# Kernel optimization log

Hardware: AMD Instinct MI355X
Metric: run time of the kernel (lower is better)

Reference implementation:

```python
import jax, jax.numpy as jnp
import numpy as np

SEQ, BATCH, HID, NLAYERS = 2048, 16, 1024, 2


def setup_inputs() -> dict:
    key = jax.random.key(0)
    ks = jax.random.split(key, 3)
    scale = 1.0 / np.sqrt(HID)
    x = jax.random.normal(ks[0], (SEQ, BATCH, HID), dtype=jnp.float32)
    W0 = jax.random.normal(ks[1], (HID, 3 * HID), dtype=jnp.float32) * scale
    b0 = jnp.zeros((2 * HID,), dtype=jnp.float32)
    W1 = jax.random.normal(ks[2], (HID, 3 * HID), dtype=jnp.float32) * scale
    b1 = jnp.zeros((2 * HID,), dtype=jnp.float32)
    return {"x": x, "W0": W0, "b0": b0, "W1": W1, "b1": b1}


def _sru_layer(x, W, b):
    # x: [L, B, H]; W: [H, 3H]; b: [2H]
    L, B, H = x.shape
    U = jnp.einsum('lbd,dk->lbk', x, W)  # [L, B, 3H]
    x_tilde = U[..., :H]
    bf, br = b[:H], b[H:]
    f = jax.nn.sigmoid(U[..., H:2 * H] + bf)  # forget gate [L,B,H]
    r = jax.nn.sigmoid(U[..., 2 * H:] + br)   # reset gate  [L,B,H]

    def step(c_prev, inp):
        xt_t, f_t = inp
        c_t = f_t * c_prev + (1.0 - f_t) * xt_t
        return c_t, c_t

    c0 = jnp.zeros((B, H), dtype=x.dtype)
    _, cs = jax.lax.scan(step, c0, (x_tilde, f))  # cs: [L, B, H]
    h = r * cs + (1.0 - r) * x  # highway connection
    return h


def reference(x, W0, b0, W1, b1):
    h = _sru_layer(x, W0, b0)
    h = _sru_layer(h, W1, b1)
    return h[-1:]  # [1, B, H], matching `out[-1:]`
```

## Files before the change

### kernel.cpp

```cpp
#include <hip/hip_runtime.h>

#define SEQ    2048
#define BATCH  16
#define HID    1024
#define M_TOT  (SEQ*BATCH)
#define NCH    (BATCH*HID)
#define NCHUNK 32
#define TCHUNK (SEQ/NCHUNK)

typedef __attribute__((ext_vector_type(8))) short          short8;
typedef __attribute__((ext_vector_type(8))) unsigned short ushort8_t;
typedef __attribute__((ext_vector_type(4))) float          floatx4;

__device__ __forceinline__ unsigned short f32_to_bf16(float f) {
  unsigned int u = __float_as_uint(f);
  u += 0x7FFFu + ((u >> 16) & 1u);
  return (unsigned short)(u >> 16);
}
__device__ __forceinline__ float bf16_to_f32(unsigned short h) {
  return __uint_as_float(((unsigned int)h) << 16);
}
__device__ __forceinline__ float sigmoidf_(float x) {
  return 1.f / (1.f + __expf(-x));
}


__device__ __forceinline__ void cast_swizzle_body(const float* __restrict__ src,
    unsigned short* __restrict__ dst, int mt, int kt, int t) {
  __shared__ unsigned short tile[4096];
  const int r = t >> 1, kh = (t & 1) * 16;
  const float* sp = src + (size_t)(mt * 128 + r) * 1024 + kt * 32 + kh;
  float4 v0 = *(const float4*)(sp + 0);
  float4 v1 = *(const float4*)(sp + 4);
  float4 v2 = *(const float4*)(sp + 8);
  float4 v3 = *(const float4*)(sp + 12);
  ushort8_t u0, u1;
  u0[0]=f32_to_bf16(v0.x); u0[1]=f32_to_bf16(v0.y); u0[2]=f32_to_bf16(v0.z); u0[3]=f32_to_bf16(v0.w);
  u0[4]=f32_to_bf16(v1.x); u0[5]=f32_to_bf16(v1.y); u0[6]=f32_to_bf16(v1.z); u0[7]=f32_to_bf16(v1.w);
  u1[0]=f32_to_bf16(v2.x); u1[1]=f32_to_bf16(v2.y); u1[2]=f32_to_bf16(v2.z); u1[3]=f32_to_bf16(v2.w);
  u1[4]=f32_to_bf16(v3.x); u1[5]=f32_to_bf16(v3.y); u1[6]=f32_to_bf16(v3.z); u1[7]=f32_to_bf16(v3.w);
  const int c = r >> 4, lr = r & 15, q0 = kh >> 3;
  const int unit0 = c * 64 + (q0 << 4) + lr;
  *(ushort8_t*)&tile[unit0 * 8]        = u0;
  *(ushort8_t*)&tile[(unit0 + 16) * 8] = u1;
  __syncthreads();
  const size_t base = ((size_t)mt * 32 + kt) * 4096;
  *(ushort8_t*)&dst[base + t * 16]     = *(const ushort8_t*)&tile[t * 16];
  *(ushort8_t*)&dst[base + t * 16 + 8] = *(const ushort8_t*)&tile[t * 16 + 8];
}

__device__ __forceinline__ void w_prep_body(const float* __restrict__ W,
    unsigned short* __restrict__ Wsw, int nt, int kt, int t) {
  __shared__ unsigned short tile[4096];
  const int kk = t >> 3, n0 = (t & 7) * 16;
  const float* sp = W + (size_t)(kt * 32 + kk) * 3072 + nt * 128 + n0;
  float v[16];
#pragma unroll
  for (int i = 0; i < 16; i += 4) {
    float4 f = *(const float4*)(sp + i);
    v[i] = f.x; v[i+1] = f.y; v[i+2] = f.z; v[i+3] = f.w;
  }
  const int cbase = (n0 >> 4) * 64 + ((kk >> 3) << 4);
#pragma unroll
  for (int j = 0; j < 16; j++)
    tile[(cbase + j) * 8 + (kk & 7)] = f32_to_bf16(v[j]);
  __syncthreads();
  const size_t base = ((size_t)nt * 32 + kt) * 4096;
  *(ushort8_t*)&Wsw[base + t * 16]     = *(const ushort8_t*)&tile[t * 16];
  *(ushort8_t*)&Wsw[base + t * 16 + 8] = *(const ushort8_t*)&tile[t * 16 + 8];
}

__global__ __launch_bounds__(256) void prep_all(const float* __restrict__ x,
    const float* __restrict__ W0, const float* __restrict__ W1,
    unsigned short* __restrict__ xsw, unsigned short* __restrict__ W0sw,
    unsigned short* __restrict__ W1sw) {
  const int id = blockIdx.x, t = threadIdx.x;
  if (id < 8192)        cast_swizzle_body(x, xsw, id >> 5, id & 31, t);
  else if (id < 8960)   w_prep_body(W0, W0sw, (id - 8192) >> 5, (id - 8192) & 31, t);
  else                  w_prep_body(W1, W1sw, (id - 8960) >> 5, (id - 8960) & 31, t);
}

__global__ __launch_bounds__(256, 2) void gemm_direct(
    const unsigned short* __restrict__ A, const unsigned short* __restrict__ B,
    unsigned short* __restrict__ Xt, unsigned short* __restrict__ Fo, unsigned short* __restrict__ Ro,
    const float* __restrict__ bias, int NBN2)
{
  const int tid = threadIdx.x;
  const int wave = tid >> 6, lane = tid & 63;
  const int wm = wave & 1, wn = wave >> 1;
  const int id = blockIdx.x;
  const int xcd = id & 7, slot = id >> 3;
  const int NB8 = NBN2 << 3;
  const int g = slot / NB8, rem = slot - g * NB8;
  const int bn = rem >> 3;
  const int bm = xcd * 32 + g * 8 + (rem & 7);

  const unsigned short* gA = A + (size_t)bm * 32 * 4096 + wm * 2048 + lane * 8;
  const unsigned short* gB = B + ((size_t)(bn * 2 + wn)) * 32 * 4096 + lane * 8;

  floatx4 acc[4][8];
#pragma unroll
  for (int i = 0; i < 4; i++)
#pragma unroll
    for (int j = 0; j < 8; j++)
#pragma unroll
      for (int r = 0; r < 4; r++) acc[i][j][r] = 0.f;

  short8 a0[4], b0[8], a1[4], b1[8];
  auto loadA = [&](short8* d, const unsigned short* p) {
#pragma unroll
    for (int i = 0; i < 4; i++) d[i] = *(const short8*)(p + i * 512);
  };
  auto loadB = [&](short8* d, const unsigned short* p) {
#pragma unroll
    for (int j = 0; j < 8; j++) d[j] = *(const short8*)(p + j * 512);
  };
  auto domfma = [&](short8* a, short8* b) {
#pragma unroll
    for (int i = 0; i < 4; i++)
#pragma unroll
      for (int j = 0; j < 8; j++)
        acc[i][j] = __builtin_amdgcn_mfma_f32_16x16x32_bf16(a[i], b[j], acc[i][j], 0, 0, 0);
  };

  loadA(a0, gA); loadB(b0, gB);
#pragma unroll 1
  for (int kt = 0; kt < 32; kt += 2) {
    loadA(a1, gA + 4096); loadB(b1, gB + 4096);
    domfma(a0, b0);
    gA += 8192; gB += 8192;
    if (kt + 2 < 32) { loadA(a0, gA); loadB(b0, gB); }
    domfma(a1, b1);
  }

  const int region = bn >> 2;
  const int lc = (bn & 3) * 256 + wn * 128 + (lane & 15);
  const int row0 = bm * 128 + wm * 64 + ((lane >> 4) << 2);
  if (region == 0) {
#pragma unroll
    for (int i = 0; i < 4; i++)
#pragma unroll
      for (int j = 0; j < 8; j++)
#pragma unroll
        for (int rg = 0; rg < 4; rg++)
          Xt[(size_t)(row0 + i * 16 + rg) * 1024 + lc + j * 16] = f32_to_bf16(acc[i][j][rg]);
  } else {
    unsigned short* O = (region == 1) ? Fo : Ro;
    const float* bp = bias + (region - 1) * 1024;
#pragma unroll
    for (int j = 0; j < 8; j++) {
      float bb = bp[lc + j * 16];
#pragma unroll
      for (int i = 0; i < 4; i++)
#pragma unroll
        for (int rg = 0; rg < 4; rg++) {
          float s = sigmoidf_(acc[i][j][rg] + bb);
          O[(size_t)(row0 + i * 16 + rg) * 1024 + lc + j * 16] = f32_to_bf16(s);
        }
    }
  }
}

__global__ __launch_bounds__(256) void scan_pass1(
    const unsigned short* __restrict__ Xt, const unsigned short* __restrict__ F,
    float* __restrict__ P, float* __restrict__ S) {
  const int ch = (blockIdx.x * 256 + threadIdx.x) * 8;
  const int chunk = blockIdx.y;
  size_t idx = (size_t)chunk * TCHUNK * NCH + ch;
  float p[8], s[8];
#pragma unroll
  for (int j = 0; j < 8; j++) { p[j] = 1.f; s[j] = 0.f; }
  for (int t = 0; t < TCHUNK; ++t) {
    ushort8_t fv = *(const ushort8_t*)&F[idx];
    ushort8_t xv = *(const ushort8_t*)&Xt[idx];
#pragma unroll
    for (int j = 0; j < 8; j++) {
      float f  = bf16_to_f32(fv[j]);
      float xt = bf16_to_f32(xv[j]);
      s[j] = f * s[j] + (1.f - f) * xt;
      p[j] *= f;
    }
    idx += NCH;
  }
  float4* P4 = (float4*)&P[(size_t)chunk * NCH + ch];
  float4* S4 = (float4*)&S[(size_t)chunk * NCH + ch];
  P4[0] = make_float4(p[0], p[1], p[2], p[3]);
  P4[1] = make_float4(p[4], p[5], p[6], p[7]);
  S4[0] = make_float4(s[0], s[1], s[2], s[3]);
  S4[1] = make_float4(s[4], s[5], s[6], s[7]);
}

__global__ __launch_bounds__(256) void combine_c0(
    const float* __restrict__ P, const float* __restrict__ S, float* __restrict__ C0) {
  const int ch = (blockIdx.x * 256 + threadIdx.x) * 8;
  float c[8];
#pragma unroll
  for (int j = 0; j < 8; j++) c[j] = 0.f;
  for (int k = 0; k < NCHUNK; ++k) {
    float4* O4 = (float4*)&C0[(size_t)k * NCH + ch];
    O4[0] = make_float4(c[0], c[1], c[2], c[3]);
    O4[1] = make_float4(c[4], c[5], c[6], c[7]);
    const float4* P4 = (const float4*)&P[(size_t)k * NCH + ch];
    const float4* S4 = (const float4*)&S[(size_t)k * NCH + ch];
    float4 p0 = P4[0], p1 = P4[1], s0 = S4[0], s1 = S4[1];
    c[0] = p0.x*c[0]+s0.x; c[1] = p0.y*c[1]+s0.y; c[2] = p0.z*c[2]+s0.z; c[3] = p0.w*c[3]+s0.w;
    c[4] = p1.x*c[4]+s1.x; c[5] = p1.y*c[5]+s1.y; c[6] = p1.z*c[6]+s1.z; c[7] = p1.w*c[7]+s1.w;
  }
}

#define TPAD 4112
__global__ __launch_bounds__(256) void scan1_pass2_fused(
    const unsigned short* __restrict__ Xt, const unsigned short* __restrict__ F,
    const unsigned short* __restrict__ R, unsigned short* __restrict__ xsw,
    const float* __restrict__ C0, unsigned short* __restrict__ h1last)
{
  __shared__ unsigned short st[4 * TPAD];
  const int hb = blockIdx.x;
  const int chunk = blockIdx.y;
  const int tid = threadIdx.x;
  const int b = tid >> 4, hg = tid & 15;
  const int h0 = hb * 128 + hg * 8;
  const int ch = b * 1024 + h0;
  const int tl   = hg >> 2;
  const int usub = (hg & 3) * 16 + b;

  float c[8];
  {
    const float4* C4 = (const float4*)&C0[(size_t)chunk * NCH + ch];
    float4 a = C4[0], d = C4[1];
    c[0]=a.x; c[1]=a.y; c[2]=a.z; c[3]=a.w; c[4]=d.x; c[5]=d.y; c[6]=d.z; c[7]=d.w;
  }

  size_t idx = (size_t)chunk * TCHUNK * NCH + ch;
  for (int t8 = 0; t8 < 8; ++t8) {
#pragma unroll
    for (int ts = 0; ts < 8; ++ts) {
      const int t = chunk * TCHUNK + t8 * 8 + ts;
      ushort8_t fv = *(const ushort8_t*)&F[idx];
      ushort8_t xv = *(const ushort8_t*)&Xt[idx];
      ushort8_t rv = *(const ushort8_t*)&R[idx];
      const size_t soff = ((size_t)(t >> 3) * 32 + (h0 >> 5)) * 4096
                        + (size_t)(((t & 7) * 64 + usub) * 8);
      ushort8_t xo = *(const ushort8_t*)&xsw[soff];
      ushort8_t hv;
#pragma unroll
      for (int j = 0; j < 8; ++j) {
        float f  = bf16_to_f32(fv[j]);
        float xt = bf16_to_f32(xv[j]);
        c[j] = f * c[j] + (1.f - f) * xt;
        float r  = bf16_to_f32(rv[j]);
        float xval = bf16_to_f32(xo[j]);
        hv[j] = f32_to_bf16(r * c[j] + (1.f - r) * xval);
      }
      *(ushort8_t*)&st[tl * TPAD + (ts * 64 + usub) * 8] = hv;
      if (t == SEQ - 1) *(ushort8_t*)&h1last[ch] = hv;
      idx += NCH;
    }
    __syncthreads();
    const size_t gbase = (((size_t)chunk * 8 + t8) * 32 + hb * 4) * 4096;
#pragma unroll
    for (int tl2 = 0; tl2 < 4; ++tl2) {
      size_t gdst = gbase + (size_t)tl2 * 4096 + tid * 16;
      *(ushort8_t*)&xsw[gdst]     = *(const ushort8_t*)&st[tl2 * TPAD + tid * 16];
      *(ushort8_t*)&xsw[gdst + 8] = *(const ushort8_t*)&st[tl2 * TPAD + tid * 16 + 8];
    }
    __syncthreads();
  }
}

__global__ __launch_bounds__(256) void r2_kernel(
    const unsigned short* __restrict__ h1last, const float* __restrict__ W1,
    const float* __restrict__ b1, float* __restrict__ r2) {
  __shared__ float xrow[1024];
  const int b = blockIdx.x, nq = blockIdx.y, tid = threadIdx.x;
  for (int i = tid; i < 1024; i += 256)
    xrow[i] = bf16_to_f32(h1last[b * 1024 + i]);
  __syncthreads();
  const int n = nq * 256 + tid;
  float acc = b1[1024 + n];
  for (int d = 0; d < 1024; ++d)
    acc += xrow[d] * W1[(size_t)d * 3072 + 2048 + n];
  r2[b * 1024 + n] = sigmoidf_(acc);
}

__global__ __launch_bounds__(256) void combine_final(
    const float* __restrict__ P, const float* __restrict__ S,
    const float* __restrict__ r2, const unsigned short* __restrict__ h1last,
    float* __restrict__ out) {
  const int ch = (blockIdx.x * 256 + threadIdx.x) * 8;
  float c[8];
#pragma unroll
  for (int j = 0; j < 8; j++) c[j] = 0.f;
  for (int k = 0; k < NCHUNK; ++k) {
    const float4* P4 = (const float4*)&P[(size_t)k * NCH + ch];
    const float4* S4 = (const float4*)&S[(size_t)k * NCH + ch];
    float4 p0 = P4[0], p1 = P4[1], s0 = S4[0], s1 = S4[1];
    c[0] = p0.x*c[0]+s0.x; c[1] = p0.y*c[1]+s0.y; c[2] = p0.z*c[2]+s0.z; c[3] = p0.w*c[3]+s0.w;
    c[4] = p1.x*c[4]+s1.x; c[5] = p1.y*c[5]+s1.y; c[6] = p1.z*c[6]+s1.z; c[7] = p1.w*c[7]+s1.w;
  }
  const float4* R4 = (const float4*)&r2[ch];
  float4 r0 = R4[0], r1 = R4[1];
  ushort8_t hx = *(const ushort8_t*)&h1last[ch];
  float o[8];
  float rr[8] = {r0.x, r0.y, r0.z, r0.w, r1.x, r1.y, r1.z, r1.w};
#pragma unroll
  for (int j = 0; j < 8; j++)
    o[j] = rr[j] * c[j] + (1.f - rr[j]) * bf16_to_f32(hx[j]);
  float4* O4 = (float4*)&out[ch];
  O4[0] = make_float4(o[0], o[1], o[2], o[3]);
  O4[1] = make_float4(o[4], o[5], o[6], o[7]);
}

extern "C" void kernel_launch(void* const* d_in, const int* in_sizes, int n_in,
                              void* d_out, int out_size, void* d_ws, size_t ws_size,
                              hipStream_t stream) {
  const float* x  = (const float*)d_in[0];
  const float* W0 = (const float*)d_in[1];
  const float* b0 = (const float*)d_in[2];
  const float* W1 = (const float*)d_in[3];
  const float* b1 = (const float*)d_in[4];
  float* out = (float*)d_out;

  char* ws = (char*)d_ws;
  auto alloc = [&](size_t bytes) {
    char* p = ws; ws += (bytes + 255) & ~(size_t)255; return p;
  };
  const size_t NE = (size_t)M_TOT * HID;
  unsigned short* xsw   = (unsigned short*)alloc(NE * 2);
  unsigned short* W0sw  = (unsigned short*)alloc((size_t)3072 * 1024 * 2);
  unsigned short* W1sw  = (unsigned short*)alloc((size_t)3072 * 1024 * 2);
  unsigned short* Xt    = (unsigned short*)alloc(NE * 2);
  unsigned short* F     = (unsigned short*)alloc(NE * 2);
  unsigned short* R     = (unsigned short*)alloc(NE * 2);
  unsigned short* h1last= (unsigned short*)alloc((size_t)NCH * 2);
  float* P   = (float*)alloc((size_t)NCHUNK * NCH * 4);
  float* S   = (float*)alloc((size_t)NCHUNK * NCH * 4);
  float* C0  = (float*)alloc((size_t)NCHUNK * NCH * 4);
  float* r2  = (float*)alloc((size_t)NCH * 4);

  dim3 blk256(256);
  prep_all<<<dim3(9728), blk256, 0, stream>>>(x, W0, W1, xsw, W0sw, W1sw);
  gemm_direct<<<dim3(256 * 12), blk256, 0, stream>>>(xsw, W0sw, Xt, F, R, b0, 12);
  scan_pass1<<<dim3(8, NCHUNK), blk256, 0, stream>>>(Xt, F, P, S);
  combine_c0<<<dim3(8), blk256, 0, stream>>>(P, S, C0);
  scan1_pass2_fused<<<dim3(8, NCHUNK), blk256, 0, stream>>>(Xt, F, R, xsw, C0, h1last);
  gemm_direct<<<dim3(256 * 8), blk256, 0, stream>>>(xsw, W1sw, Xt, F, R, b1, 8);
  r2_kernel<<<dim3(16, 4), blk256, 0, stream>>>(h1last, W1, b1, r2);
  scan_pass1<<<dim3(8, NCHUNK), blk256, 0, stream>>>(Xt, F, P, S);
  combine_final<<<dim3(8), blk256, 0, stream>>>(P, S, r2, h1last, out);
}
```

Baseline: 833.9 us.

## Fuse layer-2 GEMM with segment scan to skip storing gate tensors

Replaces the second-layer GEMM plus scan_pass1 with a kernel that computes only the x_tilde and forget-gate columns, applies the sigmoid and reduces each 32-row tile to a per-segment (product, scan) pair in registers and shared memory. This avoids writing and rereading the full Xt and F tensors. The final kernel then combines 256 segments instead of 32 chunks. The change also raises the occupancy hint on gemm_direct from 2 to 3, which may pressure registers.

```diff
diff --git a/kernel.cpp b/kernel.cpp
--- a/kernel.cpp
+++ b/kernel.cpp
@@ -7,6 +7,7 @@
 #define NCH    (BATCH*HID)
 #define NCHUNK 32
 #define TCHUNK (SEQ/NCHUNK)
+#define NSEG   256
 
 typedef __attribute__((ext_vector_type(8))) short          short8;
 typedef __attribute__((ext_vector_type(8))) unsigned short ushort8_t;
@@ -80,7 +81,7 @@
   else                  w_prep_body(W1, W1sw, (id - 8960) >> 5, (id - 8960) & 31, t);
 }
 
-__global__ __launch_bounds__(256, 2) void gemm_direct(
+__global__ __launch_bounds__(256, 3) void gemm_direct(
     const unsigned short* __restrict__ A, const unsigned short* __restrict__ B,
     unsigned short* __restrict__ Xt, unsigned short* __restrict__ Fo, unsigned short* __restrict__ Ro,
     const float* __restrict__ bias, int NBN2)
@@ -157,6 +158,102 @@
           float s = sigmoidf_(acc[i][j][rg] + bb);
           O[(size_t)(row0 + i * 16 + rg) * 1024 + lc + j * 16] = f32_to_bf16(s);
         }
+    }
+  }
+}
+
+__global__ __launch_bounds__(256, 2) void gemm2_scan(
+    const unsigned short* __restrict__ A, const unsigned short* __restrict__ B,
+    const float* __restrict__ bias, float* __restrict__ Pseg, float* __restrict__ Sseg)
+{
+  __shared__ float lps[2][64][4][4][2];
+  const int tid = threadIdx.x;
+  const int wave = tid >> 6, lane = tid & 63;
+  const int wm = wave & 1, wn = wave >> 1;
+  const int id = blockIdx.x;
+  const int xcd = id & 7, slot = id >> 3;
+  const int g = slot >> 6, rem = slot & 63;
+  const int bn = rem >> 3;
+  const int bm = xcd * 32 + g * 8 + (rem & 7);
+
+  const unsigned short* gA  = A + (size_t)bm * 32 * 4096 + wm * 2048 + lane * 8;
+  const unsigned short* gBx = B + (size_t)bn * 32 * 4096 + wn * 2048 + lane * 8;
+  const unsigned short* gBf = B + (size_t)(8 + bn) * 32 * 4096 + wn * 2048 + lane * 8;
+
+  floatx4 ax[4][4], af[4][4];
+#pragma unroll
+  for (int i = 0; i < 4; i++)
+#pragma unroll
+    for (int j = 0; j < 4; j++)
+#pragma unroll
+      for (int r = 0; r < 4; r++) { ax[i][j][r] = 0.f; af[i][j][r] = 0.f; }
+
+  short8 a0[4], bx0[4], bf0[4], a1[4], bx1[4], bf1[4];
+  auto load4 = [&](short8* d, const unsigned short* p) {
+#pragma unroll
+    for (int i = 0; i < 4; i++) d[i] = *(const short8*)(p + i * 512);
+  };
+  auto domfma = [&](short8* a, short8* bx, short8* bf) {
+#pragma unroll
+    for (int i = 0; i < 4; i++)
+#pragma unroll
+      for (int j = 0; j < 4; j++) {
+        ax[i][j] = __builtin_amdgcn_mfma_f32_16x16x32_bf16(a[i], bx[j], ax[i][j], 0, 0, 0);
+        af[i][j] = __builtin_amdgcn_mfma_f32_16x16x32_bf16(a[i], bf[j], af[i][j], 0, 0, 0);
+      }
+  };
+
+  load4(a0, gA); load4(bx0, gBx); load4(bf0, gBf);
+#pragma unroll 1
+  for (int kt = 0; kt < 32; kt += 2) {
+    load4(a1, gA + 4096); load4(bx1, gBx + 4096); load4(bf1, gBf + 4096);
+    domfma(a0, bx0, bf0);
+    gA += 8192; gBx += 8192; gBf += 8192;
+    if (kt + 2 < 32) { load4(a0, gA); load4(bx0, gBx); load4(bf0, gBf); }
+    domfma(a1, bx1, bf1);
+  }
+
+  const int q = lane >> 4, cc = lane & 15;
+  float pv[4][4], sv[4][4];
+#pragma unroll
+  for (int j = 0; j < 4; j++) {
+    float bb = bias[bn * 128 + wn * 64 + j * 16 + cc];
+#pragma unroll
+    for (int rg = 0; rg < 4; rg++) {
+      float p = 1.f, s = 0.f;
+#pragma unroll
+      for (int i = 0; i < 4; i++) {
+        float f  = sigmoidf_(af[i][j][rg] + bb);
+        float xt = ax[i][j][rg];
+        s = f * s + (1.f - f) * xt;
+        p *= f;
+      }
+      pv[j][rg] = p; sv[j][rg] = s;
+    }
+  }
+  if (wm == 0) {
+#pragma unroll
+    for (int j = 0; j < 4; j++)
+#pragma unroll
+      for (int rg = 0; rg < 4; rg++) {
+        lps[wn][lane][rg][j][0] = pv[j][rg];
+        lps[wn][lane][rg][j][1] = sv[j][rg];
+      }
+  }
+  __syncthreads();
+  if (wm == 1) {
+#pragma unroll
+    for (int j = 0; j < 4; j++) {
+      const int h = bn * 128 + wn * 64 + j * 16 + cc;
+#pragma unroll
+      for (int rg = 0; rg < 4; rg++) {
+        float plo = lps[wn][lane][rg][j][0];
+        float slo = lps[wn][lane][rg][j][1];
+        float phi = pv[j][rg], shi = sv[j][rg];
+        const size_t off = (size_t)bm * NCH + (q * 4 + rg) * 1024 + h;
+        Pseg[off] = plo * phi;
+        Sseg[off] = phi * slo + shi;
+      }
     }
   }
 }
@@ -283,17 +380,18 @@
   r2[b * 1024 + n] = sigmoidf_(acc);
 }
 
-__global__ __launch_bounds__(256) void combine_final(
-    const float* __restrict__ P, const float* __restrict__ S,
+__global__ __launch_bounds__(256) void final_l2(
+    const float* __restrict__ Pseg, const float* __restrict__ Sseg,
     const float* __restrict__ r2, const unsigned short* __restrict__ h1last,
     float* __restrict__ out) {
   const int ch = (blockIdx.x * 256 + threadIdx.x) * 8;
   float c[8];
 #pragma unroll
   for (int j = 0; j < 8; j++) c[j] = 0.f;
-  for (int k = 0; k < NCHUNK; ++k) {
-    const float4* P4 = (const float4*)&P[(size_t)k * NCH + ch];
-    const float4* S4 = (const float4*)&S[(size_t)k * NCH + ch];
+#pragma unroll 4
+  for (int k = 0; k < NSEG; ++k) {
+    const float4* P4 = (const float4*)&Pseg[(size_t)k * NCH + ch];
+    const float4* S4 = (const float4*)&Sseg[(size_t)k * NCH + ch];
     float4 p0 = P4[0], p1 = P4[1], s0 = S4[0], s1 = S4[1];
     c[0] = p0.x*c[0]+s0.x; c[1] = p0.y*c[1]+s0.y; c[2] = p0.z*c[2]+s0.z; c[3] = p0.w*c[3]+s0.w;
     c[4] = p1.x*c[4]+s1.x; c[5] = p1.y*c[5]+s1.y; c[6] = p1.z*c[6]+s1.z; c[7] = p1.w*c[7]+s1.w;
@@ -301,8 +399,8 @@
   const float4* R4 = (const float4*)&r2[ch];
   float4 r0 = R4[0], r1 = R4[1];
   ushort8_t hx = *(const ushort8_t*)&h1last[ch];
+  float rr[8] = {r0.x, r0.y, r0.z, r0.w, r1.x, r1.y, r1.z, r1.w};
   float o[8];
-  float rr[8] = {r0.x, r0.y, r0.z, r0.w, r1.x, r1.y, r1.z, r1.w};
 #pragma unroll
   for (int j = 0; j < 8; j++)
     o[j] = rr[j] * c[j] + (1.f - rr[j]) * bf16_to_f32(hx[j]);
@@ -333,10 +431,12 @@
   unsigned short* F     = (unsigned short*)alloc(NE * 2);
   unsigned short* R     = (unsigned short*)alloc(NE * 2);
   unsigned short* h1last= (unsigned short*)alloc((size_t)NCH * 2);
-  float* P   = (float*)alloc((size_t)NCHUNK * NCH * 4);
-  float* S   = (float*)alloc((size_t)NCHUNK * NCH * 4);
-  float* C0  = (float*)alloc((size_t)NCHUNK * NCH * 4);
-  float* r2  = (float*)alloc((size_t)NCH * 4);
+  float* P    = (float*)alloc((size_t)NCHUNK * NCH * 4);
+  float* S    = (float*)alloc((size_t)NCHUNK * NCH * 4);
+  float* C0   = (float*)alloc((size_t)NCHUNK * NCH * 4);
+  float* Pseg = (float*)alloc((size_t)NSEG * NCH * 4);
+  float* Sseg = (float*)alloc((size_t)NSEG * NCH * 4);
+  float* r2   = (float*)alloc((size_t)NCH * 4);
 
   dim3 blk256(256);
   prep_all<<<dim3(9728), blk256, 0, stream>>>(x, W0, W1, xsw, W0sw, W1sw);
@@ -344,8 +444,7 @@
   scan_pass1<<<dim3(8, NCHUNK), blk256, 0, stream>>>(Xt, F, P, S);
   combine_c0<<<dim3(8), blk256, 0, stream>>>(P, S, C0);
   scan1_pass2_fused<<<dim3(8, NCHUNK), blk256, 0, stream>>>(Xt, F, R, xsw, C0, h1last);
-  gemm_direct<<<dim3(256 * 8), blk256, 0, stream>>>(xsw, W1sw, Xt, F, R, b1, 8);
   r2_kernel<<<dim3(16, 4), blk256, 0, stream>>>(h1last, W1, b1, r2);
-  scan_pass1<<<dim3(8, NCHUNK), blk256, 0, stream>>>(Xt, F, P, S);
-  combine_final<<<dim3(8), blk256, 0, stream>>>(P, S, r2, h1last, out);
-}
+  gemm2_scan<<<dim3(2048), blk256, 0, stream>>>(xsw, W1sw, b1, Pseg, Sseg);
+  final_l2<<<dim3(8), blk256, 0, stream>>>(Pseg, Sseg, r2, h1last, out);
+}
```

Measured after the change: 2.108 ms. 153% more time.
